# Kernel optimization log

Measured on AMD Instinct MI355X. Metric: run time of the kernel, lower is better.

The kernel has to match this reference:

```python
import jax, jax.numpy as jnp
import numpy as np

B, T, C, H = 4, 2048, 1024, 16
D = C // H  # head_dim = 64


def setup_inputs() -> dict:
    key = jax.random.key(0)
    k1, k2, k3, k4, k5 = jax.random.split(key, 5)
    x = jax.random.normal(k1, (B, T, C), dtype=jnp.float32)
    # torch nn.Linear weights: [out_features, in_features]
    s = 1.0 / np.sqrt(C)
    qkv_w = jax.random.uniform(k2, (3 * C, C), dtype=jnp.float32, minval=-s, maxval=s)
    qkv_b = jax.random.uniform(k3, (3 * C,), dtype=jnp.float32, minval=-s, maxval=s)
    out_w = jax.random.uniform(k4, (C, C), dtype=jnp.float32, minval=-s, maxval=s)
    out_b = jax.random.uniform(k5, (C,), dtype=jnp.float32, minval=-s, maxval=s)
    # causal mask broadcastable to [B,H,T,T]; 0 (False) marks masked positions
    attn_mask = jnp.tril(jnp.ones((T, T), dtype=bool))[None, None]
    return {"x": x, "qkv_w": qkv_w, "qkv_b": qkv_b, "out_w": out_w,
            "out_b": out_b, "attn_mask": attn_mask}


def reference(x, qkv_w, qkv_b, out_w, out_b, attn_mask):
    qkv = x @ qkv_w.T + qkv_b                      # [B,T,3C]
    q, k, v = jnp.split(qkv, 3, axis=-1)
    # [B,T,C] -> [B,H,T,D]
    q = q.reshape(B, T, H, D).transpose(0, 2, 1, 3)
    k = k.reshape(B, T, H, D).transpose(0, 2, 1, 3)
    v = v.reshape(B, T, H, D).transpose(0, 2, 1, 3)
    scale = 1.0 / np.sqrt(D)
    attn = jnp.einsum('bhqd,bhkd->bhqk', q, k) * scale   # [B,H,T,T]
    neg = jnp.finfo(attn.dtype).min
    attn = jnp.where(attn_mask, attn, neg)
    attn = jax.nn.softmax(attn, axis=-1)
    out = jnp.einsum('bhqk,bhkd->bhqd', attn, v)          # [B,H,T,D]
    out = out.transpose(0, 2, 1, 3).reshape(B, T, C)
    return out @ out_w.T + out_b
```

## Files before the change

### kernel.cpp

```cpp
#include <hip/hip_runtime.h>
#include <hip/hip_bf16.h>
#include <math.h>

#define B_ 4
#define T_ 2048
#define C_ 1024
#define H_ 16
#define D_ 64

typedef __hip_bfloat16 bf16;
typedef float f32x4 __attribute__((ext_vector_type(4)));
typedef short bf16s8 __attribute__((ext_vector_type(8)));

#define NEG_BIG (-1e30f)
#define QSCALE 0.18033688011112042f

__device__ inline unsigned short f2bf(float f) {
  __hip_bfloat16 h = __float2bfloat16(f);
  return *reinterpret_cast<unsigned short*>(&h);
}
__device__ inline float bf_lo(unsigned u) {
  union { unsigned u; float f; } c; c.u = u << 16; return c.f;
}

__device__ inline void async_load16(const void* g, void* l) {
  __builtin_amdgcn_global_load_lds(
      (const __attribute__((address_space(1))) unsigned int*)g,
      (__attribute__((address_space(3))) unsigned int*)l, 16, 0, 0);
}

union U4 { uint4 u; unsigned short s[8]; };

__device__ inline uint4 load8(const void* base, size_t idx, int f32) {
  if (f32) {
    const float* p = (const float*)base + idx;
    float4 a = *(const float4*)p;
    float4 b = *(const float4*)(p + 4);
    U4 r;
    r.s[0] = f2bf(a.x); r.s[1] = f2bf(a.y); r.s[2] = f2bf(a.z); r.s[3] = f2bf(a.w);
    r.s[4] = f2bf(b.x); r.s[5] = f2bf(b.y); r.s[6] = f2bf(b.z); r.s[7] = f2bf(b.w);
    return r.u;
  }
  return *(const uint4*)((const unsigned short*)base + idx);
}

#define R_X   1048576
#define R_WQ  (R_X + 393216)
#define R_WO  (R_WQ + 131072)
#define R_BQ  (R_WO + 384)
#define R_BO  (R_BQ + 128)
__global__ __launch_bounds__(256) void convert_all_k(
    const void* __restrict__ x, const void* __restrict__ wq,
    const void* __restrict__ wo, const void* __restrict__ bq,
    const void* __restrict__ bo,
    bf16* __restrict__ xd, bf16* __restrict__ wqd, bf16* __restrict__ wod,
    bf16* __restrict__ bqd, bf16* __restrict__ bod,
    int* __restrict__ flag) {
  __shared__ int sany[4];
  const int tid = threadIdx.x;
  {
    const unsigned short* w = (const unsigned short*)wq;
    float f0 = bf_lo((unsigned)w[tid * 2]);
    float f1 = bf_lo((unsigned)w[tid * 2 + 1]);
    bool big = !(fabsf(f0) <= 1.0f) || !(fabsf(f1) <= 1.0f);
    int any = __any(big);
    if ((tid & 63) == 0) sany[tid >> 6] = any;
  }
  __syncthreads();
  const int f32 = (sany[0] | sany[1] | sany[2] | sany[3]) ? 1 : 0;

  long long g = (long long)blockIdx.x * 256 + tid;
  if (g == 0) *flag = f32;
  if (g >= R_BO) return;
  const void* src; bf16* dst; long long base;
  if (g < R_X)       { src = x;  dst = xd;  base = 0; }
  else if (g < R_WQ) { src = wq; dst = wqd; base = R_X; }
  else if (g < R_WO) { src = wo; dst = wod; base = R_WQ; }
  else if (g < R_BQ) { src = bq; dst = bqd; base = R_WO; }
  else               { src = bo; dst = bod; base = R_BQ; }
  size_t i = (size_t)(g - base) * 8;
  *(uint4*)(dst + i) = load8(src, i, f32);
}

template <int KDIM, int MROWS>
__device__ inline void gemm_core(const bf16* __restrict__ A,
                                 const bf16* __restrict__ W,
                                 int tm, int tn, int wm, int wn,
                                 f32x4 acc[MROWS / 32][4], bf16* As, bf16* Bs) {
  const int tid  = threadIdx.x;
  const int lane = tid & 63;
  const int rl   = lane & 15;
  const int kq   = (lane >> 4) * 8;

  for (int k0 = 0; k0 < KDIM; k0 += 32) {
    __syncthreads();
#pragma unroll
    for (int j = 0; j < MROWS / 64; ++j) {
      int f    = j * 4096 + tid * 16;
      int row  = f >> 6;
      int colb = f & 63;
      async_load16((const char*)A + ((size_t)(tm + row) * KDIM + k0) * 2 + colb,
                   (char*)As + f);
    }
#pragma unroll
    for (int j = 0; j < 2; ++j) {
      int f    = j * 4096 + tid * 16;
      int row  = f >> 6;
      int colb = f & 63;
      async_load16((const char*)W + ((size_t)(tn + row) * KDIM + k0) * 2 + colb,
                   (char*)Bs + f);
    }
    __syncthreads();

    bf16s8 af[MROWS / 32], bw[4];
#pragma unroll
    for (int mt = 0; mt < MROWS / 32; ++mt)
      af[mt] = *(const bf16s8*)(As + (wm + mt * 16 + rl) * 32 + kq);
#pragma unroll
    for (int nt = 0; nt < 4; ++nt)
      bw[nt] = *(const bf16s8*)(Bs + (wn + nt * 16 + rl) * 32 + kq);

#pragma unroll
    for (int mt = 0; mt < MROWS / 32; ++mt)
#pragma unroll
      for (int nt = 0; nt < 4; ++nt)
        acc[mt][nt] = __builtin_amdgcn_mfma_f32_16x16x32_bf16(af[mt], bw[nt],
                                                              acc[mt][nt], 0, 0, 0);
  }
}

#define CSTRIDE 72
#define FSTRIDE 68

__global__ __launch_bounds__(256) void gemm_qkv_k(
    const bf16* __restrict__ X, const bf16* __restrict__ W,
    const bf16* __restrict__ bias,
    bf16* __restrict__ q, bf16* __restrict__ k, bf16* __restrict__ v) {
  __shared__ __align__(16) char smem[4 * 64 * CSTRIDE * 2];
  bf16* As = (bf16*)smem;
  bf16* Bs = (bf16*)(smem + 8192);
  const int tid = threadIdx.x;
  const int wave = tid >> 6, lane = tid & 63;
  const int tm = blockIdx.x * 128, tn = blockIdx.y * 128;
  const int wm = (wave >> 1) * 64, wn = (wave & 1) * 64;
  f32x4 acc[4][4];
#pragma unroll
  for (int i = 0; i < 4; ++i)
#pragma unroll
    for (int j = 0; j < 4; ++j) acc[i][j] = 0.0f;

  gemm_core<C_, 128>(X, W, tm, tn, wm, wn, acc, As, Bs);

  __syncthreads();
  bf16* Cs = (bf16*)smem + wave * 64 * CSTRIDE;

  const int rl = lane & 15, qd = lane >> 4;
  const int nbase = tn + wn;
  const int which = nbase >> 10;
  const int h = (nbase & 1023) >> 6;
  const int mbase = tm + wm;
  const int b = mbase >> 11, t0 = mbase & 2047;

  if (which == 2) {
#pragma unroll
    for (int nt = 0; nt < 4; ++nt) {
      float bv = __bfloat162float(bias[nbase + nt * 16 + rl]);
#pragma unroll
      for (int mt = 0; mt < 4; ++mt)
#pragma unroll
        for (int r = 0; r < 4; ++r)
          Cs[(nt * 16 + rl) * CSTRIDE + 32 * (mt >> 1) + 8 * qd + 4 * (mt & 1) + r] =
              __float2bfloat16(acc[mt][nt][r] + bv);
    }
    bf16* vbase = v + ((size_t)(b * H_ + h) * D_) * T_ + t0;
#pragma unroll
    for (int it = 0; it < 8; ++it) {
      int row = it * 8 + (lane >> 3);
      uint4 val = *(const uint4*)(Cs + row * CSTRIDE + (lane & 7) * 8);
      *(uint4*)(vbase + (size_t)row * T_ + (lane & 7) * 8) = val;
    }
  } else {
    const float sc = which == 0 ? QSCALE : 1.0f;
    bf16* dst = which == 0 ? q : k;
    bf16* base = dst + (((size_t)(b * H_ + h)) * T_ + t0) * D_;
#pragma unroll
    for (int nt = 0; nt < 4; ++nt) {
      float bv = __bfloat162float(bias[nbase + nt * 16 + rl]);
#pragma unroll
      for (int mt = 0; mt < 4; ++mt)
#pragma unroll
        for (int r = 0; r < 4; ++r)
          Cs[(mt * 16 + qd * 4 + r) * CSTRIDE + nt * 16 + rl] =
              __float2bfloat16((acc[mt][nt][r] + bv) * sc);
    }
#pragma unroll
    for (int it = 0; it < 8; ++it) {
      int row = it * 8 + (lane >> 3);
      uint4 val = *(const uint4*)(Cs + row * CSTRIDE + (lane & 7) * 8);
      *(uint4*)(base + row * D_ + (lane & 7) * 8) = val;
    }
  }
}

__global__ __launch_bounds__(256) void gemm_out_k(
    const bf16* __restrict__ O, const bf16* __restrict__ W,
    const bf16* __restrict__ bias, const int* __restrict__ flag,
    void* __restrict__ out) {
  __shared__ __align__(16) char smem[4 * 64 * CSTRIDE * 2];
  bf16* As = (bf16*)smem;
  bf16* Bs = (bf16*)(smem + 8192);
  const int f32 = *flag;
  const int tid = threadIdx.x;
  const int wave = tid >> 6, lane = tid & 63;
  const int tm = blockIdx.x * 128, tn = blockIdx.y * 128;
  const int wm = (wave >> 1) * 64, wn = (wave & 1) * 64;
  f32x4 acc[4][4];
#pragma unroll
  for (int i = 0; i < 4; ++i)
#pragma unroll
    for (int j = 0; j < 4; ++j) acc[i][j] = 0.0f;

  gemm_core<C_, 128>(O, W, tm, tn, wm, wn, acc, As, Bs);

  __syncthreads();
  const int rl = lane & 15, qd = lane >> 4;

  if (f32) {
    float* Cs = (float*)smem + wave * 32 * FSTRIDE;
#pragma unroll
    for (int pass = 0; pass < 2; ++pass) {
#pragma unroll
      for (int nt = 0; nt < 4; ++nt) {
        float bv = __bfloat162float(bias[tn + wn + nt * 16 + rl]);
#pragma unroll
        for (int mt = 0; mt < 2; ++mt)
#pragma unroll
          for (int r = 0; r < 4; ++r)
            Cs[(mt * 16 + qd * 4 + r) * FSTRIDE + nt * 16 + rl] =
                acc[pass * 2 + mt][nt][r] + bv;
      }
      float* obase = (float*)out + (size_t)(tm + wm + pass * 32) * C_ + tn + wn;
#pragma unroll
      for (int it = 0; it < 8; ++it) {
        int row = it * 4 + (lane >> 4);
        float4 val = *(const float4*)(Cs + row * FSTRIDE + (lane & 15) * 4);
        *(float4*)(obase + (size_t)row * C_ + (lane & 15) * 4) = val;
      }
    }
  } else {
    bf16* Cs = (bf16*)smem + wave * 64 * CSTRIDE;
#pragma unroll
    for (int nt = 0; nt < 4; ++nt) {
      float bv = __bfloat162float(bias[tn + wn + nt * 16 + rl]);
#pragma unroll
      for (int mt = 0; mt < 4; ++mt)
#pragma unroll
        for (int r = 0; r < 4; ++r)
          Cs[(mt * 16 + qd * 4 + r) * CSTRIDE + nt * 16 + rl] =
              __float2bfloat16(acc[mt][nt][r] + bv);
    }
    bf16* obase = (bf16*)out + (size_t)(tm + wm) * C_ + tn + wn;
#pragma unroll
    for (int it = 0; it < 8; ++it) {
      int row = it * 8 + (lane >> 3);
      uint4 val = *(const uint4*)(Cs + row * CSTRIDE + (lane & 7) * 8);
      *(uint4*)(obase + (size_t)row * C_ + (lane & 7) * 8) = val;
    }
  }
}

__global__ __launch_bounds__(256) void fattn_k(
    const bf16* __restrict__ q, const bf16* __restrict__ k,
    const bf16* __restrict__ vT, bf16* __restrict__ o) {
  __shared__ __align__(16) bf16 Ks[2][64 * 64];
  __shared__ __align__(16) bf16 Vs[2][64 * 64];
  const int tid = threadIdx.x, wave = tid >> 6, lane = tid & 63;
  const int rl = lane & 15, quad = lane >> 4;
  const int bh = blockIdx.x;
  const int b = bh >> 4, h = bh & 15;
  const size_t bhT = (size_t)bh * T_;
  const int sw0 = (quad ^ (rl & 7)) << 3;
  const int sw1 = ((quad | 4) ^ (rl & 7)) << 3;

  bf16s8 ones;
#pragma unroll
  for (int i = 0; i < 8; ++i) ones[i] = (short)0x3F80;

  const int qb = 31 - blockIdx.y;
  const int q0 = qb * 64;

  const int kr0 = tid >> 3;
  const int kc0 = ((tid & 7) ^ (kr0 & 7)) << 4;
  const char* kstage = (const char*)k + (bhT + kr0) * (D_ * 2) + kc0;
  const char* vstage = (const char*)vT + ((size_t)bh * D_ + kr0) * (T_ * 2) + kc0;

  const bf16* qr = q + (bhT + q0 + wave * 16 + rl) * D_;
  bf16s8 qf0 = *(const bf16s8*)(qr + quad * 8);
  bf16s8 qf1 = *(const bf16s8*)(qr + 32 + quad * 8);

  f32x4 oacc[4], lacc;
#pragma unroll
  for (int nt = 0; nt < 4; ++nt) oacc[nt] = 0.0f;
  lacc = 0.0f;

  const int nchunk = qb + 1;

  {
    char* kd = (char*)Ks[0] + tid * 16;
    async_load16(kstage, kd);
    async_load16(kstage + 4096, kd + 4096);
    char* vd = (char*)Vs[0] + tid * 16;
    async_load16(vstage, vd);
    async_load16(vstage + 131072, vd + 4096);
  }
  __syncthreads();

  int cur = 0;
#pragma unroll 1
  for (int c = 0; c < nchunk; ++c) {
    const bf16* Kc = Ks[cur];
    const bf16* Vc = Vs[cur];
    const bool pf = (c + 1 < nchunk);

    if (pf) {
      const size_t ak = (size_t)(c + 1) * 8192;
      char* kd = (char*)Ks[cur ^ 1] + tid * 16;
      async_load16(kstage + ak, kd);
      async_load16(kstage + ak + 4096, kd + 4096);
      const size_t av = (size_t)(c + 1) * 128;
      char* vd = (char*)Vs[cur ^ 1] + tid * 16;
      async_load16(vstage + av, vd);
      async_load16(vstage + av + 131072, vd + 4096);
    }

    const int t0 = q0 + wave * 16;
    const int k0 = c << 6;

    f32x4 s[4];
#pragma unroll
    for (int nt = 0; nt < 4; ++nt) s[nt] = 0.0f;
    __builtin_amdgcn_s_setprio(1);
#pragma unroll
    for (int nt = 0; nt < 4; ++nt) {
      int key = nt * 16 + rl;
      bf16s8 kb0 = *(const bf16s8*)(Kc + key * 64 + sw0);
      bf16s8 kb1 = *(const bf16s8*)(Kc + key * 64 + sw1);
      s[nt] = __builtin_amdgcn_mfma_f32_16x16x32_bf16(kb0, qf0, s[nt], 0, 0, 0);
      s[nt] = __builtin_amdgcn_mfma_f32_16x16x32_bf16(kb1, qf1, s[nt], 0, 0, 0);
    }
    __builtin_amdgcn_s_setprio(0);

    if (c == nchunk - 1) {
      int t = t0 + rl;
#pragma unroll
      for (int nt = 0; nt < 4; ++nt)
#pragma unroll
        for (int r = 0; r < 4; ++r) {
          int key = k0 + nt * 16 + quad * 4 + r;
          if (key > t) s[nt][r] = NEG_BIG;
        }
    }

    unsigned pk[4][2];
#pragma unroll
    for (int nt = 0; nt < 4; ++nt) {
#pragma unroll
      for (int r = 0; r < 4; ++r)
        s[nt][r] = __builtin_amdgcn_exp2f(s[nt][r]);
      pk[nt][0] = (unsigned)f2bf(s[nt][0]) | ((unsigned)f2bf(s[nt][1]) << 16);
      pk[nt][1] = (unsigned)f2bf(s[nt][2]) | ((unsigned)f2bf(s[nt][3]) << 16);
    }
    union { unsigned w[4]; bf16s8 v; } A0, A1;
    A0.w[0] = pk[0][0]; A0.w[1] = pk[0][1]; A0.w[2] = pk[1][0]; A0.w[3] = pk[1][1];
    A1.w[0] = pk[2][0]; A1.w[1] = pk[2][1]; A1.w[2] = pk[3][0]; A1.w[3] = pk[3][1];

    __builtin_amdgcn_s_setprio(1);
    lacc = __builtin_amdgcn_mfma_f32_16x16x32_bf16(A0.v, ones, lacc, 0, 0, 0);
    lacc = __builtin_amdgcn_mfma_f32_16x16x32_bf16(A1.v, ones, lacc, 0, 0, 0);
#pragma unroll
    for (int nt = 0; nt < 4; ++nt) {
      int d = nt * 16 + rl;
      bf16s8 vb0 = *(const bf16s8*)(Vc + d * 64 + sw0);
      bf16s8 vb1 = *(const bf16s8*)(Vc + d * 64 + sw1);
      oacc[nt] = __builtin_amdgcn_mfma_f32_16x16x32_bf16(A0.v, vb0, oacc[nt], 0, 0, 0);
      oacc[nt] = __builtin_amdgcn_mfma_f32_16x16x32_bf16(A1.v, vb1, oacc[nt], 0, 0, 0);
    }
    __builtin_amdgcn_s_setprio(0);

    __syncthreads();
    cur ^= 1;
  }

  f32x4 linv;
#pragma unroll
  for (int r = 0; r < 4; ++r) linv[r] = 1.0f / lacc[r];
#pragma unroll
  for (int nt = 0; nt < 4; ++nt) {
    int d = nt * 16 + rl;
#pragma unroll
    for (int r = 0; r < 4; ++r) {
      int t = q0 + wave * 16 + quad * 4 + r;
      o[((size_t)b * T_ + t) * C_ + h * D_ + d] =
          __float2bfloat16(oacc[nt][r] * linv[r]);
    }
  }
}

extern "C" void kernel_launch(void* const* d_in, const int* in_sizes, int n_in,
                              void* d_out, int out_size, void* d_ws, size_t ws_size,
                              hipStream_t stream) {
  (void)in_sizes; (void)n_in; (void)out_size; (void)ws_size;
  const void* x     = d_in[0];
  const void* qkv_w = d_in[1];
  const void* qkv_b = d_in[2];
  const void* out_w = d_in[3];
  const void* out_b = d_in[4];

  const size_t nqkv = (size_t)B_ * T_ * C_;
  char* ws = (char*)d_ws;
  int*  flag = (int*)ws;
  bf16* q   = (bf16*)(ws + 256);
  bf16* kk  = q + nqkv;
  bf16* vv  = kk + nqkv;
  bf16* oo  = vv + nqkv;
  bf16* xbf = oo;
  bf16* wqkv = oo + nqkv;
  bf16* wout = wqkv + 3 * C_ * C_;
  bf16* bqkv = wout + C_ * C_;
  bf16* bout = bqkv + 3 * C_;

  convert_all_k<<<(R_BO + 255) / 256, 256, 0, stream>>>(
      x, qkv_w, out_w, qkv_b, out_b, xbf, wqkv, wout, bqkv, bout, flag);

  gemm_qkv_k<<<dim3(64, 24), 256, 0, stream>>>(xbf, wqkv, bqkv, q, kk, vv);
  fattn_k<<<dim3(64, 32), 256, 0, stream>>>(q, kk, vv, oo);
  gemm_out_k<<<dim3(64, 8), 256, 0, stream>>>(oo, wout, bout, flag, d_out);
}
```

Measured before the change: 253.0 us.

## Double GEMM K-tile to 64 and XOR-swizzle shared-memory tiles

The shared GEMM core now stages a 64-wide K slice of A and W per iteration instead of 32. This halves the number of barrier-separated load/compute rounds and gives each wave twice as many MFMAs per sync. Tiles are stored with an XOR swizzle on 16-byte column groups keyed by row, so the per-lane fragment reads avoid LDS bank conflicts. The B tile offset moves to fit the larger A tile within the existing shared buffer, and register pressure rises from holding two K-halves of fragments.

After: 248.9 us. Within noise of the previous version (-1.6%).

```diff
diff --git a/kernel.cpp b/kernel.cpp
--- a/kernel.cpp
+++ b/kernel.cpp
@@ -90,42 +90,49 @@
   const int tid  = threadIdx.x;
   const int lane = tid & 63;
   const int rl   = lane & 15;
-  const int kq   = (lane >> 4) * 8;
-
-  for (int k0 = 0; k0 < KDIM; k0 += 32) {
+  const int quad = lane >> 4;
+
+  const int r0  = tid >> 3;
+  const int cg0 = ((tid & 7) ^ (r0 & 7)) << 4;
+
+  for (int k0 = 0; k0 < KDIM; k0 += 64) {
     __syncthreads();
 #pragma unroll
-    for (int j = 0; j < MROWS / 64; ++j) {
-      int f    = j * 4096 + tid * 16;
-      int row  = f >> 6;
-      int colb = f & 63;
-      async_load16((const char*)A + ((size_t)(tm + row) * KDIM + k0) * 2 + colb,
-                   (char*)As + f);
-    }
-#pragma unroll
-    for (int j = 0; j < 2; ++j) {
-      int f    = j * 4096 + tid * 16;
-      int row  = f >> 6;
-      int colb = f & 63;
-      async_load16((const char*)W + ((size_t)(tn + row) * KDIM + k0) * 2 + colb,
-                   (char*)Bs + f);
-    }
+    for (int j = 0; j < MROWS / 32; ++j)
+      async_load16((const char*)A + ((size_t)(tm + j * 32 + r0) * KDIM + k0) * 2 + cg0,
+                   (char*)As + j * 4096 + tid * 16);
+#pragma unroll
+    for (int j = 0; j < 4; ++j)
+      async_load16((const char*)W + ((size_t)(tn + j * 32 + r0) * KDIM + k0) * 2 + cg0,
+                   (char*)Bs + j * 4096 + tid * 16);
     __syncthreads();
 
-    bf16s8 af[MROWS / 32], bw[4];
-#pragma unroll
-    for (int mt = 0; mt < MROWS / 32; ++mt)
-      af[mt] = *(const bf16s8*)(As + (wm + mt * 16 + rl) * 32 + kq);
-#pragma unroll
-    for (int nt = 0; nt < 4; ++nt)
-      bw[nt] = *(const bf16s8*)(Bs + (wn + nt * 16 + rl) * 32 + kq);
-
-#pragma unroll
-    for (int mt = 0; mt < MROWS / 32; ++mt)
-#pragma unroll
-      for (int nt = 0; nt < 4; ++nt)
-        acc[mt][nt] = __builtin_amdgcn_mfma_f32_16x16x32_bf16(af[mt], bw[nt],
-                                                              acc[mt][nt], 0, 0, 0);
+    bf16s8 af[MROWS / 32][2], bw[4][2];
+#pragma unroll
+    for (int mt = 0; mt < MROWS / 32; ++mt) {
+      int row = wm + mt * 16 + rl;
+#pragma unroll
+      for (int kk = 0; kk < 2; ++kk)
+        af[mt][kk] = *(const bf16s8*)(As + row * 64 +
+                                      (((kk * 4 + quad) ^ (row & 7)) << 3));
+    }
+#pragma unroll
+    for (int nt = 0; nt < 4; ++nt) {
+      int row = wn + nt * 16 + rl;
+#pragma unroll
+      for (int kk = 0; kk < 2; ++kk)
+        bw[nt][kk] = *(const bf16s8*)(Bs + row * 64 +
+                                      (((kk * 4 + quad) ^ (row & 7)) << 3));
+    }
+
+#pragma unroll
+    for (int kk = 0; kk < 2; ++kk)
+#pragma unroll
+      for (int mt = 0; mt < MROWS / 32; ++mt)
+#pragma unroll
+        for (int nt = 0; nt < 4; ++nt)
+          acc[mt][nt] = __builtin_amdgcn_mfma_f32_16x16x32_bf16(
+              af[mt][kk], bw[nt][kk], acc[mt][nt], 0, 0, 0);
   }
 }
 
@@ -138,7 +145,7 @@
     bf16* __restrict__ q, bf16* __restrict__ k, bf16* __restrict__ v) {
   __shared__ __align__(16) char smem[4 * 64 * CSTRIDE * 2];
   bf16* As = (bf16*)smem;
-  bf16* Bs = (bf16*)(smem + 8192);
+  bf16* Bs = (bf16*)(smem + 16384);
   const int tid = threadIdx.x;
   const int wave = tid >> 6, lane = tid & 63;
   const int tm = blockIdx.x * 128, tn = blockIdx.y * 128;
@@ -208,7 +215,7 @@
     void* __restrict__ out) {
   __shared__ __align__(16) char smem[4 * 64 * CSTRIDE * 2];
   bf16* As = (bf16*)smem;
-  bf16* Bs = (bf16*)(smem + 8192);
+  bf16* Bs = (bf16*)(smem + 16384);
   const int f32 = *flag;
   const int tid = threadIdx.x;
   const int wave = tid >> 6, lane = tid & 63;
```
